# Kernel tuning notes

Measured on AMD Instinct MI355X. Metric: run time of the kernel, lower is better.

## Reference

```python
import jax, jax.numpy as jnp
import numpy as np

B, IMG, PATCH = 32, 128, 8
D, H, L, MLP, NC = 512, 8, 8, 2048, 3
P = (IMG // PATCH) ** 2  # 256 patches
N = P + 1                # +cls token
HD = D // H


def layer_norm(x, g, b, eps=1e-5):
    mu = jnp.mean(x, -1, keepdims=True)
    var = jnp.mean((x - mu) ** 2, -1, keepdims=True)
    return (x - mu) * jax.lax.rsqrt(var + eps) * g + b


def spt(x, w, b, g, beta):
    s = 1
    shifts = [x,
              jnp.roll(x, (s, s), (2, 3)),
              jnp.roll(x, (-s, s), (2, 3)),
              jnp.roll(x, (s, -s), (2, 3)),
              jnp.roll(x, (-s, -s), (2, 3))]
    xs = jnp.concatenate(shifts, axis=1)  # (B,5,H,W)
    y = jax.lax.conv_general_dilated(
        xs, w, (PATCH, PATCH), 'VALID',
        dimension_numbers=('NCHW', 'OIHW', 'NCHW')) + b[None, :, None, None]
    tok = y.reshape(y.shape[0], D, -1).transpose(0, 2, 1)  # (B,P,D)
    return layer_norm(tok, g, beta)


def block(tok, p):
    ln1g, ln1b, qkvw, qkvb, projw, projb, temp, ln2g, ln2b, w1, b1, w2, b2 = p
    x = layer_norm(tok, ln1g, ln1b)
    qkv = (x @ qkvw + qkvb).reshape(x.shape[0], N, 3, H, HD)
    q = jnp.transpose(qkv[:, :, 0], (0, 2, 1, 3))  # (B,H,N,HD)
    k = jnp.transpose(qkv[:, :, 1], (0, 2, 1, 3))
    v = jnp.transpose(qkv[:, :, 2], (0, 2, 1, 3))
    attn = jnp.einsum('bhnd,bhmd->bhnm', q, k) * temp[None, :, None, None]
    attn = jnp.where(jnp.eye(N, dtype=bool)[None, None], -jnp.inf, attn)
    attn = jax.nn.softmax(attn, -1)
    o = jnp.einsum('bhnm,bhmd->bhnd', attn, v)
    o = jnp.transpose(o, (0, 2, 1, 3)).reshape(x.shape[0], N, D)
    tok = tok + o @ projw + projb
    y = layer_norm(tok, ln2g, ln2b)
    y = jax.nn.gelu(y @ w1 + b1, approximate=False) @ w2 + b2
    return tok + y


def setup_inputs() -> dict:
    key = jax.random.key(0)
    ks = jax.random.split(key, 16)
    sc = 0.02
    inp = dict(
        image=jax.random.uniform(ks[0], (B, 1, IMG, IMG), jnp.float32),
        ssw=jax.random.normal(ks[1], (D, 5, PATCH, PATCH), jnp.float32) * sc,
        ssb=jnp.zeros((D,), jnp.float32),
        ssg=jnp.ones((D,), jnp.float32),
        ssbeta=jnp.zeros((D,), jnp.float32),
        sow=jax.random.normal(ks[2], (D, 5, PATCH, PATCH), jnp.float32) * sc,
        sob=jnp.zeros((D,), jnp.float32),
        sog=jnp.ones((D,), jnp.float32),
        sobeta=jnp.zeros((D,), jnp.float32),
        fw=jax.random.normal(ks[3], (2 * D, D), jnp.float32) * sc,
        fb=jnp.zeros((D,), jnp.float32),
        cls_token=jax.random.normal(ks[4], (1, 1, D), jnp.float32) * sc,
        pos_embed=jax.random.normal(ks[5], (1, N, D), jnp.float32) * sc,
        ln1g=jnp.ones((L, D), jnp.float32),
        ln1b=jnp.zeros((L, D), jnp.float32),
        qkvw=jax.random.normal(ks[6], (L, D, 3 * D), jnp.float32) * sc,
        qkvb=jnp.zeros((L, 3 * D), jnp.float32),
        projw=jax.random.normal(ks[7], (L, D, D), jnp.float32) * sc,
        projb=jnp.zeros((L, D), jnp.float32),
        temp=jnp.ones((L, H), jnp.float32) / np.sqrt(HD),
        ln2g=jnp.ones((L, D), jnp.float32),
        ln2b=jnp.zeros((L, D), jnp.float32),
        w1=jax.random.normal(ks[8], (L, D, MLP), jnp.float32) * sc,
        b1=jnp.zeros((L, MLP), jnp.float32),
        w2=jax.random.normal(ks[9], (L, MLP, D), jnp.float32) * sc,
        b2=jnp.zeros((L, D), jnp.float32),
        ng=jnp.ones((D,), jnp.float32),
        nb=jnp.zeros((D,), jnp.float32),
        hw=jax.random.normal(ks[10], (D, NC), jnp.float32) * sc,
        hb=jnp.zeros((NC,), jnp.float32),
    )
    return inp


def reference(image, ssw, ssb, ssg, ssbeta, sow, sob, sog, sobeta, fw, fb,
              cls_token, pos_embed, ln1g, ln1b, qkvw, qkvb, projw, projb,
              temp, ln2g, ln2b, w1, b1, w2, b2, ng, nb, hw, hb):
    # InverseLensLayer is undefined in the source repo snippet: identity
    source = image
    src_tok = spt(source, ssw, ssb, ssg, ssbeta)   # (B,P,D)
    orig_tok = spt(image, sow, sob, sog, sobeta)   # (B,P,D)
    comb = jnp.concatenate([src_tok, orig_tok], -1)
    gate = jax.nn.sigmoid(comb @ fw + fb)
    fused = gate * src_tok + (1.0 - gate) * orig_tok
    cls = jnp.broadcast_to(cls_token, (image.shape[0], 1, D))
    tokens = jnp.concatenate([cls, fused], axis=1) + pos_embed  # (B,N,D)

    def body(tok, p):
        return block(tok, p), None

    params = (ln1g, ln1b, qkvw, qkvb, projw, projb, temp,
              ln2g, ln2b, w1, b1, w2, b2)
    tokens, _ = jax.lax.scan(body, tokens, params)
    cls_out = layer_norm(tokens[:, 0], ng, nb)
    logits = cls_out @ hw + hb
    return logits
```

## Files before the change

kernel.cpp:

```cpp
#include <hip/hip_runtime.h>
#include <math.h>

constexpr int B_ = 32, D_ = 512, H_ = 8, L_ = 8, MLP_ = 2048, NC_ = 3;
constexpr int P_ = 256;
constexpr int N_ = 257;
constexpr int HD_ = 64;
constexpr int BP_ = B_ * P_;
constexpr int BN_ = B_ * N_;
constexpr int MP_ = 8320;
constexpr int KP_ = 320;
constexpr int NV_ = 288;

enum { EPI_BIAS = 0, EPI_RES = 1, EPI_GELU = 2 };

using bf16x8 = __attribute__((ext_vector_type(8))) short;
using f32x4  = __attribute__((ext_vector_type(4))) float;

__device__ __forceinline__ float b2f(unsigned short u) {
    return __uint_as_float(((unsigned)u) << 16);
}
__device__ __forceinline__ unsigned short f2b(float f) {
    unsigned u = __float_as_uint(f);
    unsigned r = (u + 0x7FFFu + ((u >> 16) & 1u)) >> 16;
    return (unsigned short)r;
}

__device__ __forceinline__ void gld_lds16(const void* g, void* l) {
    __builtin_amdgcn_global_load_lds(
        (const __attribute__((address_space(1))) void*)g,
        (__attribute__((address_space(3))) void*)l, 16, 0, 0);
}

__global__ void im2col_k(const float* __restrict__ img,
                         unsigned short* __restrict__ X) {
    int idx = blockIdx.x * 256 + threadIdx.x;
    if (idx >= BP_ * KP_) return;
    int r = idx / KP_, j = idx % KP_;
    int b = r >> 8, p = r & 255;
    int py = p >> 4, px = p & 15;
    int c = j >> 6, kk = j & 63;
    int ky = kk >> 3, kx = kk & 7;
    const int dy[5] = {0, 1, -1, 1, -1};
    const int dx[5] = {0, 1, 1, -1, -1};
    int yy = (py * 8 + ky - dy[c] + 128) & 127;
    int xx = (px * 8 + kx - dx[c] + 128) & 127;
    X[idx] = f2b(img[b * 16384 + yy * 128 + xx]);
}

__global__ __launch_bounds__(256) void castT_k(const float* __restrict__ in,
                                               unsigned short* __restrict__ out,
                                               int K, int N) {
    __shared__ float t[32][33];
    size_t loff = (size_t)blockIdx.z * K * N;
    int k0 = blockIdx.x * 32, n0 = blockIdx.y * 32;
    int tx = threadIdx.x & 31, ty = threadIdx.x >> 5;
    for (int i = ty; i < 32; i += 8)
        t[i][tx] = in[loff + (size_t)(k0 + i) * N + n0 + tx];
    __syncthreads();
    for (int i = ty; i < 32; i += 8)
        out[loff + (size_t)(n0 + i) * K + k0 + tx] = f2b(t[tx][i]);
}

__global__ void cast_k(const float* __restrict__ in,
                       unsigned short* __restrict__ out, int n) {
    int idx = blockIdx.x * 256 + threadIdx.x;
    if (idx < n) out[idx] = f2b(in[idx]);
}

template <int TNT, int NTHR>
__global__ __launch_bounds__(NTHR) void gemm2_k(
    const unsigned short* __restrict__ A, const unsigned short* __restrict__ Bt,
    const float* __restrict__ bias, const float* __restrict__ res,
    float* __restrict__ outF, unsigned short* __restrict__ outB,
    int Nn, int K, int epi) {
    constexpr int BK = 64;
    constexpr int NW = NTHR / 64;
    constexpr int NWC = NW / 2;
    constexpr int ACH = 128 * 8;
    constexpr int BCH = TNT * 8;
    __shared__ unsigned short As[128 * BK];
    __shared__ unsigned short Bs[TNT * BK];
    int tid = threadIdx.x, lane = tid & 63, wave = tid >> 6;
    int quad = lane >> 4, cid = lane & 15;
    int wrow = (wave / NWC) * 64, wcol = (wave % NWC) * 64;
    size_t bm = (size_t)blockIdx.y * 128, bn = (size_t)blockIdx.x * TNT;
    const unsigned short* Ab = A + bm * K;
    const unsigned short* Bb = Bt + bn * K;

    f32x4 acc[4][4] = {};

    for (int k0 = 0; k0 < K; k0 += BK) {
#pragma unroll
        for (int c0 = 0; c0 < ACH; c0 += NTHR) {
            int c = c0 + tid;
            int row = c >> 3, j = c & 7;
            int k8 = j ^ (row & 7);
            int cw = c0 + (tid & ~63);
            gld_lds16(Ab + (size_t)row * K + k0 + k8 * 8,
                      (char*)As + cw * 16);
        }
#pragma unroll
        for (int c0 = 0; c0 < BCH; c0 += NTHR) {
            int c = c0 + tid;
            int row = c >> 3, j = c & 7;
            int k8 = j ^ (row & 7);
            int cw = c0 + (tid & ~63);
            gld_lds16(Bb + (size_t)row * K + k0 + k8 * 8,
                      (char*)Bs + cw * 16);
        }
        __syncthreads();
#pragma unroll
        for (int ks = 0; ks < 2; ++ks) {
            bf16x8 af[4], bfr[4];
#pragma unroll
            for (int i = 0; i < 4; ++i) {
                int r = wrow + i * 16 + cid;
                int j = (ks * 4 + quad) ^ (r & 7);
                af[i] = *(const bf16x8*)&As[(r * 8 + j) * 8];
            }
#pragma unroll
            for (int i = 0; i < 4; ++i) {
                int r = wcol + i * 16 + cid;
                int j = (ks * 4 + quad) ^ (r & 7);
                bfr[i] = *(const bf16x8*)&Bs[(r * 8 + j) * 8];
            }
#pragma unroll
            for (int mi = 0; mi < 4; ++mi)
#pragma unroll
                for (int ni = 0; ni < 4; ++ni)
                    acc[mi][ni] = __builtin_amdgcn_mfma_f32_16x16x32_bf16(
                        af[mi], bfr[ni], acc[mi][ni], 0, 0, 0);
        }
        __syncthreads();
    }

#pragma unroll
    for (int mi = 0; mi < 4; ++mi) {
#pragma unroll
        for (int ni = 0; ni < 4; ++ni) {
            size_t gm0 = bm + wrow + mi * 16 + quad * 4;
            size_t gn = bn + wcol + ni * 16 + cid;
            float bs = bias ? bias[gn] : 0.f;
#pragma unroll
            for (int r = 0; r < 4; ++r) {
                size_t o = (gm0 + r) * Nn + gn;
                float v = acc[mi][ni][r] + bs;
                if (epi == EPI_GELU)
                    v = 0.5f * v * (1.f + erff(v * 0.70710678118654752f));
                else if (epi == EPI_RES)
                    v += res[o];
                if (outF) outF[o] = v;
                if (outB) outB[o] = f2b(v);
            }
        }
    }
}

__global__ __launch_bounds__(256) void ln_k(
    const float* __restrict__ in, float* __restrict__ outF,
    unsigned short* __restrict__ outB, const float* __restrict__ g,
    const float* __restrict__ be, long instride, long ofs, long obs) {
    __shared__ float red[256];
    int row = blockIdx.x;
    const float* x = in + (size_t)row * instride;
    int t = threadIdx.x;
    float v0 = x[t], v1 = x[t + 256];
    red[t] = v0 + v1;
    __syncthreads();
    for (int s = 128; s > 0; s >>= 1) {
        if (t < s) red[t] += red[t + s];
        __syncthreads();
    }
    float mu = red[0] * (1.f / 512.f);
    __syncthreads();
    float d0 = v0 - mu, d1 = v1 - mu;
    red[t] = d0 * d0 + d1 * d1;
    __syncthreads();
    for (int s = 128; s > 0; s >>= 1) {
        if (t < s) red[t] += red[t + s];
        __syncthreads();
    }
    float rs = rsqrtf(red[0] * (1.f / 512.f) + 1e-5f);
    float y0 = d0 * rs * g[t] + be[t];
    float y1 = d1 * rs * g[t + 256] + be[t + 256];
    if (outF) {
        float* y = outF + (size_t)row * ofs;
        y[t] = y0; y[t + 256] = y1;
    }
    if (outB) {
        unsigned short* y = outB + (size_t)row * obs;
        y[t] = f2b(y0); y[t + 256] = f2b(y1);
    }
}

__global__ void assemble_k(const float* __restrict__ gatelin,
                           const float* __restrict__ src,
                           const float* __restrict__ orig,
                           const float* __restrict__ cls,
                           const float* __restrict__ pos,
                           float* __restrict__ tokens) {
    int idx = blockIdx.x * 256 + threadIdx.x;
    if (idx >= B_ * N_ * D_) return;
    int d = idx & 511;
    int bn = idx >> 9;
    int b = bn / N_, n = bn % N_;
    float v;
    if (n == 0) {
        v = cls[d];
    } else {
        int r = b * 256 + (n - 1);
        float gl = gatelin[r * 512 + d];
        float g = 1.f / (1.f + expf(-gl));
        v = g * src[r * 512 + d] + (1.f - g) * orig[r * 512 + d];
    }
    tokens[idx] = v + pos[n * 512 + d];
}

__global__ __launch_bounds__(256) void vT_k(const unsigned short* __restrict__ qkv,
                                            unsigned short* __restrict__ Vt_g) {
    __shared__ unsigned short t[64][72];
    int bh = blockIdx.x, nt = blockIdx.y;
    int b = bh >> 3, h = bh & 7;
    int n0 = nt * 64;
    const unsigned short* vb = qkv + (size_t)(b * N_) * 1536 + 1024 + h * 64;
    int tid = threadIdx.x;
    for (int idx = tid; idx < 64 * 8; idx += 256) {
        int n = idx >> 3, c = idx & 7;
        int gn = n0 + n;
        uint4 u = {0, 0, 0, 0};
        if (gn < N_) u = *(const uint4*)(vb + (size_t)gn * 1536 + c * 8);
        *(uint4*)&t[n][c * 8] = u;
    }
    __syncthreads();
    for (int idx = tid; idx < 64 * 8; idx += 256) {
        int d = idx >> 3, j = idx & 7;
        if (n0 + j * 8 >= NV_) continue;
        unsigned short tmp[8];
#pragma unroll
        for (int e = 0; e < 8; ++e) tmp[e] = t[j * 8 + e][d];
        *(uint4*)&Vt_g[((size_t)bh * 64 + d) * NV_ + n0 + j * 8] =
            *(uint4*)tmp;
    }
}

__global__ __launch_bounds__(256) void attn_fused_k(
    const unsigned short* __restrict__ qkv,
    const unsigned short* __restrict__ Vt_g, const float* __restrict__ temp,
    unsigned short* __restrict__ obuf) {
    __shared__ __align__(16) unsigned short Ps[4][16][40];
    int bh = blockIdx.x;
    int b = bh >> 3, h = bh & 7;
    int tid = threadIdx.x, lane = tid & 63, wave = tid >> 6;
    int quad = lane >> 4, cid = lane & 15;
    int qt = blockIdx.y * 4 + wave;
    if (qt > 16) return;
    const unsigned short* qb = qkv + (size_t)(b * N_) * 1536 + h * 64;
    const unsigned short* kb = qb + 512;
    const unsigned short* vt = Vt_g + (size_t)bh * 64 * NV_;
    float tmp = temp[h];

    int qrow = qt * 16 + cid;
    if (qrow > 256) qrow = 256;
    bf16x8 aq0 = *(const bf16x8*)(qb + (size_t)qrow * 1536 + quad * 8);
    bf16x8 aq1 = *(const bf16x8*)(qb + (size_t)qrow * 1536 + 32 + quad * 8);

    f32x4 s[18];
#pragma unroll
    for (int t = 0; t < 17; ++t) {
        int krow = t * 16 + cid;
        if (t == 16 && krow > 256) krow = 256;
        const unsigned short* kp = kb + (size_t)krow * 1536 + quad * 8;
        bf16x8 bk0 = *(const bf16x8*)kp;
        bf16x8 bk1 = *(const bf16x8*)(kp + 32);
        f32x4 a = {0.f, 0.f, 0.f, 0.f};
        a = __builtin_amdgcn_mfma_f32_16x16x32_bf16(aq0, bk0, a, 0, 0, 0);
        a = __builtin_amdgcn_mfma_f32_16x16x32_bf16(aq1, bk1, a, 0, 0, 0);
        s[t] = a;
    }

    float mx[4] = {-1e30f, -1e30f, -1e30f, -1e30f};
#pragma unroll
    for (int t = 0; t < 17; ++t) {
        int col = t * 16 + cid;
#pragma unroll
        for (int r = 0; r < 4; ++r) {
            int row = qt * 16 + quad * 4 + r;
            float v = s[t][r] * tmp;
            if (col == row || col >= 257) v = -1e30f;
            s[t][r] = v;
            mx[r] = fmaxf(mx[r], v);
        }
    }
    s[17] = f32x4{-1e30f, -1e30f, -1e30f, -1e30f};
#pragma unroll
    for (int m = 1; m < 16; m <<= 1)
#pragma unroll
        for (int r = 0; r < 4; ++r) mx[r] = fmaxf(mx[r], __shfl_xor(mx[r], m));
    float sum[4] = {0.f, 0.f, 0.f, 0.f};
#pragma unroll
    for (int t = 0; t < 18; ++t)
#pragma unroll
        for (int r = 0; r < 4; ++r) {
            float e = __expf(s[t][r] - mx[r]);
            float ef = b2f(f2b(e));
            s[t][r] = ef;
            sum[r] += ef;
        }
#pragma unroll
    for (int m = 1; m < 16; m <<= 1)
#pragma unroll
        for (int r = 0; r < 4; ++r) sum[r] += __shfl_xor(sum[r], m);
    float inv[4];
#pragma unroll
    for (int r = 0; r < 4; ++r) inv[r] = 1.f / sum[r];

    f32x4 o[4] = {};
#pragma unroll
    for (int kt = 0; kt < 9; ++kt) {
#pragma unroll
        for (int hh = 0; hh < 2; ++hh) {
            int t = kt * 2 + hh;
#pragma unroll
            for (int r = 0; r < 4; ++r)
                Ps[wave][quad * 4 + r][hh * 16 + cid] = f2b(s[t][r]);
        }
        bf16x8 ap = *(const bf16x8*)&Ps[wave][cid][quad * 8];
#pragma unroll
        for (int dt = 0; dt < 4; ++dt) {
            bf16x8 bv = *(const bf16x8*)(vt + (size_t)(dt * 16 + cid) * NV_ +
                                         kt * 32 + quad * 8);
            o[dt] =
                __builtin_amdgcn_mfma_f32_16x16x32_bf16(ap, bv, o[dt], 0, 0, 0);
        }
    }
#pragma unroll
    for (int dt = 0; dt < 4; ++dt)
#pragma unroll
        for (int r = 0; r < 4; ++r) {
            int row = qt * 16 + quad * 4 + r;
            if (row < N_)
                obuf[(size_t)(b * N_ + row) * 512 + h * 64 + dt * 16 + cid] =
                    f2b(o[dt][r] * inv[r]);
        }
}

__global__ void head_k(const float* __restrict__ cls_out,
                       const float* __restrict__ hw,
                       const float* __restrict__ hb, float* __restrict__ out) {
    int t = threadIdx.x;
    if (t >= B_ * NC_) return;
    int b = t / NC_, c = t % NC_;
    float acc = hb[c];
    for (int d = 0; d < D_; ++d) acc += cls_out[b * D_ + d] * hw[d * NC_ + c];
    out[t] = acc;
}

extern "C" void kernel_launch(void* const* d_in, const int* in_sizes, int n_in,
                              void* d_out, int out_size, void* d_ws,
                              size_t ws_size, hipStream_t stream) {
    const float* image     = (const float*)d_in[0];
    const float* ssw       = (const float*)d_in[1];
    const float* ssb       = (const float*)d_in[2];
    const float* ssg       = (const float*)d_in[3];
    const float* ssbeta    = (const float*)d_in[4];
    const float* sow       = (const float*)d_in[5];
    const float* sob       = (const float*)d_in[6];
    const float* sog       = (const float*)d_in[7];
    const float* sobeta    = (const float*)d_in[8];
    const float* fw        = (const float*)d_in[9];
    const float* fb        = (const float*)d_in[10];
    const float* cls_token = (const float*)d_in[11];
    const float* pos_embed = (const float*)d_in[12];
    const float* ln1g      = (const float*)d_in[13];
    const float* ln1b      = (const float*)d_in[14];
    const float* qkvw      = (const float*)d_in[15];
    const float* qkvb      = (const float*)d_in[16];
    const float* projw     = (const float*)d_in[17];
    const float* projb     = (const float*)d_in[18];
    const float* temp      = (const float*)d_in[19];
    const float* ln2g      = (const float*)d_in[20];
    const float* ln2b      = (const float*)d_in[21];
    const float* w1        = (const float*)d_in[22];
    const float* b1        = (const float*)d_in[23];
    const float* w2        = (const float*)d_in[24];
    const float* b2        = (const float*)d_in[25];
    const float* ng        = (const float*)d_in[26];
    const float* nb        = (const float*)d_in[27];
    const float* hw        = (const float*)d_in[28];
    const float* hb        = (const float*)d_in[29];
    float* out = (float*)d_out;

    char* w = (char*)d_ws;
    size_t off = 0;
    float* tokens = (float*)w;                           off += (size_t)MP_ * 512 * 4;
    unsigned short* qkvw_t = (unsigned short*)(w + off); off += (size_t)8 * 1536 * 512 * 2;
    unsigned short* projw_t = (unsigned short*)(w + off); off += (size_t)8 * 512 * 512 * 2;
    unsigned short* w1_t = (unsigned short*)(w + off);   off += (size_t)8 * 2048 * 512 * 2;
    unsigned short* w2_t = (unsigned short*)(w + off);   off += (size_t)8 * 512 * 2048 * 2;
    unsigned short* fw_t = (unsigned short*)(w + off);   off += (size_t)512 * 1024 * 2;
    unsigned short* sswb = (unsigned short*)(w + off);   off += (size_t)512 * 320 * 2;
    unsigned short* sowb = (unsigned short*)(w + off);   off += (size_t)512 * 320 * 2;
    char* S = w + off;

    unsigned short* Xb   = (unsigned short*)S;
    float* srct          = (float*)(S + 5242880);
    float* origt         = (float*)(S + 5242880 + 16777216);
    unsigned short* comb = (unsigned short*)(S + 5242880 + 2 * 16777216);
    float* gatelin       = (float*)(S + 5242880 + 3 * 16777216);

    unsigned short* xbuf = (unsigned short*)S;
    unsigned short* qkvB = (unsigned short*)(S + 8519680);
    unsigned short* obuf = (unsigned short*)(S + 8519680 + 25559040);
    unsigned short* hbuf = (unsigned short*)(S + 8519680 + 25559040 + 8519680);
    unsigned short* vt_g = (unsigned short*)(S + 8519680 + 25559040 + 8519680 +
                                             34078720);
    float* cls_out = (float*)(S + 8519680 + 25559040 + 8519680 + 34078720 +
                              9437184);

    castT_k<<<dim3(16, 48, 8), 256, 0, stream>>>(qkvw, qkvw_t, 512, 1536);
    castT_k<<<dim3(16, 16, 8), 256, 0, stream>>>(projw, projw_t, 512, 512);
    castT_k<<<dim3(16, 64, 8), 256, 0, stream>>>(w1, w1_t, 512, 2048);
    castT_k<<<dim3(64, 16, 8), 256, 0, stream>>>(w2, w2_t, 2048, 512);
    castT_k<<<dim3(32, 16, 1), 256, 0, stream>>>(fw, fw_t, 1024, 512);
    cast_k<<<640, 256, 0, stream>>>(ssw, sswb, 512 * 320);
    cast_k<<<640, 256, 0, stream>>>(sow, sowb, 512 * 320);

    im2col_k<<<(BP_ * KP_ + 255) / 256, 256, 0, stream>>>(image, Xb);
    dim3 gspt(4, 64);
    gemm2_k<128, 256><<<gspt, 256, 0, stream>>>(Xb, sswb, ssb, nullptr, srct,
                                                nullptr, 512, KP_, EPI_BIAS);
    ln_k<<<BP_, 256, 0, stream>>>(srct, srct, comb, ssg, ssbeta, 512, 512, 1024);
    gemm2_k<128, 256><<<gspt, 256, 0, stream>>>(Xb, sowb, sob, nullptr, origt,
                                                nullptr, 512, KP_, EPI_BIAS);
    ln_k<<<BP_, 256, 0, stream>>>(origt, origt, comb + 512, sog, sobeta, 512,
                                  512, 1024);
    gemm2_k<128, 256><<<gspt, 256, 0, stream>>>(comb, fw_t, fb, nullptr,
                                                gatelin, nullptr, 512, 1024,
                                                EPI_BIAS);
    assemble_k<<<(B_ * N_ * D_ + 255) / 256, 256, 0, stream>>>(
        gatelin, srct, origt, cls_token, pos_embed, tokens);

    dim3 gqkv(6, 65), gproj(4, 65), gfc1(8, 65), gfc2(4, 65);
    for (int l = 0; l < L_; ++l) {
        const float* l1g = ln1g + l * D_;
        const float* l1b = ln1b + l * D_;
        const unsigned short* qw = qkvw_t + (size_t)l * 1536 * 512;
        const float* qb  = qkvb + (size_t)l * 3 * D_;
        const unsigned short* pw = projw_t + (size_t)l * 512 * 512;
        const float* pb  = projb + (size_t)l * D_;
        const float* tp  = temp + l * H_;
        const float* l2g = ln2g + l * D_;
        const float* l2b = ln2b + l * D_;
        const unsigned short* w1l = w1_t + (size_t)l * 2048 * 512;
        const float* b1l = b1 + (size_t)l * MLP_;
        const unsigned short* w2l = w2_t + (size_t)l * 512 * 2048;
        const float* b2l = b2 + (size_t)l * D_;

        ln_k<<<BN_, 256, 0, stream>>>(tokens, nullptr, xbuf, l1g, l1b, 512, 0,
                                      512);
        gemm2_k<256, 512><<<gqkv, 512, 0, stream>>>(xbuf, qw, qb, nullptr,
                                                    nullptr, qkvB, 1536, 512,
                                                    EPI_BIAS);
        vT_k<<<dim3(256, 5), 256, 0, stream>>>(qkvB, vt_g);
        attn_fused_k<<<dim3(256, 5), 256, 0, stream>>>(qkvB, vt_g, tp, obuf);
        gemm2_k<128, 256><<<gproj, 256, 0, stream>>>(obuf, pw, pb, tokens,
                                                     tokens, nullptr, 512, 512,
                                                     EPI_RES);
        ln_k<<<BN_, 256, 0, stream>>>(tokens, nullptr, xbuf, l2g, l2b, 512, 0,
                                      512);
        gemm2_k<256, 512><<<gfc1, 512, 0, stream>>>(xbuf, w1l, b1l, nullptr,
                                                    nullptr, hbuf, 2048, 512,
                                                    EPI_GELU);
        gemm2_k<128, 256><<<gfc2, 256, 0, stream>>>(hbuf, w2l, b2l, tokens,
                                                    tokens, nullptr, 512, 2048,
                                                    EPI_RES);
    }

    ln_k<<<B_, 256, 0, stream>>>(tokens, cls_out, nullptr, ng, nb,
                                 (long)N_ * 512, 512, 0);
    head_k<<<1, 128, 0, stream>>>(cls_out, hw, hb, out);
}
```

Baseline: 2.559 ms.

## Double-buffer LDS tiles in GEMM and unify on 128x128 tile kernel

Replaces the templated single-buffered GEMM with a 128x128-tile kernel that double-buffers A/B tiles in shared memory, issuing the next tile's global-to-LDS loads before computing the current one and needing only one barrier per k-step. The QKV and FC1 GEMMs move from 256-wide tiles with 512 threads to 128-wide tiles with 256 threads, which doubles their grid sizes. Shared memory per block grows to 64KB, which may limit occupancy. The smaller tiles also give less reuse per block.

```diff
diff --git a/kernel.cpp b/kernel.cpp
--- a/kernel.cpp
+++ b/kernel.cpp
@@ -67,72 +67,84 @@
     if (idx < n) out[idx] = f2b(in[idx]);
 }
 
-template <int TNT, int NTHR>
-__global__ __launch_bounds__(NTHR) void gemm2_k(
+__device__ __forceinline__ void stage_tile(const unsigned short* __restrict__ Ab,
+                                           const unsigned short* __restrict__ Bb,
+                                           int K, int k0,
+                                           unsigned short* As,
+                                           unsigned short* Bs, int tid) {
+#pragma unroll
+    for (int c0 = 0; c0 < 1024; c0 += 256) {
+        int c = c0 + tid;
+        int row = c >> 3, j = c & 7;
+        int k8 = j ^ (row & 7);
+        int cw = c0 + (tid & ~63);
+        gld_lds16(Ab + (size_t)row * K + k0 + k8 * 8, (char*)As + cw * 16);
+    }
+#pragma unroll
+    for (int c0 = 0; c0 < 1024; c0 += 256) {
+        int c = c0 + tid;
+        int row = c >> 3, j = c & 7;
+        int k8 = j ^ (row & 7);
+        int cw = c0 + (tid & ~63);
+        gld_lds16(Bb + (size_t)row * K + k0 + k8 * 8, (char*)Bs + cw * 16);
+    }
+}
+
+__device__ __forceinline__ void compute_tile(const unsigned short* As,
+                                             const unsigned short* Bs,
+                                             int wrow, int wcol, int cid,
+                                             int quad, f32x4 acc[4][4]) {
+#pragma unroll
+    for (int ks = 0; ks < 2; ++ks) {
+        bf16x8 af[4], bfr[4];
+#pragma unroll
+        for (int i = 0; i < 4; ++i) {
+            int r = wrow + i * 16 + cid;
+            int j = (ks * 4 + quad) ^ (r & 7);
+            af[i] = *(const bf16x8*)&As[(r * 8 + j) * 8];
+        }
+#pragma unroll
+        for (int i = 0; i < 4; ++i) {
+            int r = wcol + i * 16 + cid;
+            int j = (ks * 4 + quad) ^ (r & 7);
+            bfr[i] = *(const bf16x8*)&Bs[(r * 8 + j) * 8];
+        }
+#pragma unroll
+        for (int mi = 0; mi < 4; ++mi)
+#pragma unroll
+            for (int ni = 0; ni < 4; ++ni)
+                acc[mi][ni] = __builtin_amdgcn_mfma_f32_16x16x32_bf16(
+                    af[mi], bfr[ni], acc[mi][ni], 0, 0, 0);
+    }
+}
+
+__global__ __launch_bounds__(256) void gemm3_k(
     const unsigned short* __restrict__ A, const unsigned short* __restrict__ Bt,
     const float* __restrict__ bias, const float* __restrict__ res,
     float* __restrict__ outF, unsigned short* __restrict__ outB,
     int Nn, int K, int epi) {
-    constexpr int BK = 64;
-    constexpr int NW = NTHR / 64;
-    constexpr int NWC = NW / 2;
-    constexpr int ACH = 128 * 8;
-    constexpr int BCH = TNT * 8;
-    __shared__ unsigned short As[128 * BK];
-    __shared__ unsigned short Bs[TNT * BK];
+    __shared__ unsigned short As[2][128 * 64];
+    __shared__ unsigned short Bs[2][128 * 64];
     int tid = threadIdx.x, lane = tid & 63, wave = tid >> 6;
     int quad = lane >> 4, cid = lane & 15;
-    int wrow = (wave / NWC) * 64, wcol = (wave % NWC) * 64;
-    size_t bm = (size_t)blockIdx.y * 128, bn = (size_t)blockIdx.x * TNT;
+    int wrow = (wave >> 1) * 64, wcol = (wave & 1) * 64;
+    size_t bm = (size_t)blockIdx.y * 128, bn = (size_t)blockIdx.x * 128;
     const unsigned short* Ab = A + bm * K;
     const unsigned short* Bb = Bt + bn * K;
 
     f32x4 acc[4][4] = {};
-
-    for (int k0 = 0; k0 < K; k0 += BK) {
-#pragma unroll
-        for (int c0 = 0; c0 < ACH; c0 += NTHR) {
-            int c = c0 + tid;
-            int row = c >> 3, j = c & 7;
-            int k8 = j ^ (row & 7);
-            int cw = c0 + (tid & ~63);
-            gld_lds16(Ab + (size_t)row * K + k0 + k8 * 8,
-                      (char*)As + cw * 16);
-        }
-#pragma unroll
-        for (int c0 = 0; c0 < BCH; c0 += NTHR) {
-            int c = c0 + tid;
-            int row = c >> 3, j = c & 7;
-            int k8 = j ^ (row & 7);
-            int cw = c0 + (tid & ~63);
-            gld_lds16(Bb + (size_t)row * K + k0 + k8 * 8,
-                      (char*)Bs + cw * 16);
-        }
+    int nst = K >> 6;
+
+    stage_tile(Ab, Bb, K, 0, As[0], Bs[0], tid);
+    __syncthreads();
+    for (int i = 0; i + 1 < nst; ++i) {
+        int cur = i & 1, nxt = cur ^ 1;
+        stage_tile(Ab, Bb, K, (i + 1) << 6, As[nxt], Bs[nxt], tid);
+        compute_tile(As[cur], Bs[cur], wrow, wcol, cid, quad, acc);
         __syncthreads();
-#pragma unroll
-        for (int ks = 0; ks < 2; ++ks) {
-            bf16x8 af[4], bfr[4];
-#pragma unroll
-            for (int i = 0; i < 4; ++i) {
-                int r = wrow + i * 16 + cid;
-                int j = (ks * 4 + quad) ^ (r & 7);
-                af[i] = *(const bf16x8*)&As[(r * 8 + j) * 8];
-            }
-#pragma unroll
-            for (int i = 0; i < 4; ++i) {
-                int r = wcol + i * 16 + cid;
-                int j = (ks * 4 + quad) ^ (r & 7);
-                bfr[i] = *(const bf16x8*)&Bs[(r * 8 + j) * 8];
-            }
-#pragma unroll
-            for (int mi = 0; mi < 4; ++mi)
-#pragma unroll
-                for (int ni = 0; ni < 4; ++ni)
-                    acc[mi][ni] = __builtin_amdgcn_mfma_f32_16x16x32_bf16(
-                        af[mi], bfr[ni], acc[mi][ni], 0, 0, 0);
-        }
-        __syncthreads();
-    }
+    }
+    compute_tile(As[(nst - 1) & 1], Bs[(nst - 1) & 1], wrow, wcol, cid, quad,
+                 acc);
 
 #pragma unroll
     for (int mi = 0; mi < 4; ++mi) {
@@ -427,20 +439,19 @@
 
     im2col_k<<<(BP_ * KP_ + 255) / 256, 256, 0, stream>>>(image, Xb);
     dim3 gspt(4, 64);
-    gemm2_k<128, 256><<<gspt, 256, 0, stream>>>(Xb, sswb, ssb, nullptr, srct,
-                                                nullptr, 512, KP_, EPI_BIAS);
+    gemm3_k<<<gspt, 256, 0, stream>>>(Xb, sswb, ssb, nullptr, srct, nullptr,
+                                      512, KP_, EPI_BIAS);
     ln_k<<<BP_, 256, 0, stream>>>(srct, srct, comb, ssg, ssbeta, 512, 512, 1024);
-    gemm2_k<128, 256><<<gspt, 256, 0, stream>>>(Xb, sowb, sob, nullptr, origt,
-                                                nullptr, 512, KP_, EPI_BIAS);
+    gemm3_k<<<gspt, 256, 0, stream>>>(Xb, sowb, sob, nullptr, origt, nullptr,
+                                      512, KP_, EPI_BIAS);
     ln_k<<<BP_, 256, 0, stream>>>(origt, origt, comb + 512, sog, sobeta, 512,
                                   512, 1024);
-    gemm2_k<128, 256><<<gspt, 256, 0, stream>>>(comb, fw_t, fb, nullptr,
-                                                gatelin, nullptr, 512, 1024,
-                                                EPI_BIAS);
+    gemm3_k<<<gspt, 256, 0, stream>>>(comb, fw_t, fb, nullptr, gatelin, nullptr,
+                                      512, 1024, EPI_BIAS);
     assemble_k<<<(B_ * N_ * D_ + 255) / 256, 256, 0, stream>>>(
         gatelin, srct, origt, cls_token, pos_embed, tokens);
 
-    dim3 gqkv(6, 65), gproj(4, 65), gfc1(8, 65), gfc2(4, 65);
+    dim3 gqkv(12, 65), gproj(4, 65), gfc1(16, 65), gfc2(4, 65);
     for (int l = 0; l < L_; ++l) {
         const float* l1g = ln1g + l * D_;
         const float* l1b = ln1b + l * D_;
@@ -458,22 +469,18 @@
 
         ln_k<<<BN_, 256, 0, stream>>>(tokens, nullptr, xbuf, l1g, l1b, 512, 0,
                                       512);
-        gemm2_k<256, 512><<<gqkv, 512, 0, stream>>>(xbuf, qw, qb, nullptr,
-                                                    nullptr, qkvB, 1536, 512,
-                                                    EPI_BIAS);
+        gemm3_k<<<gqkv, 256, 0, stream>>>(xbuf, qw, qb, nullptr, nullptr, qkvB,
+                                          1536, 512, EPI_BIAS);
         vT_k<<<dim3(256, 5), 256, 0, stream>>>(qkvB, vt_g);
         attn_fused_k<<<dim3(256, 5), 256, 0, stream>>>(qkvB, vt_g, tp, obuf);
-        gemm2_k<128, 256><<<gproj, 256, 0, stream>>>(obuf, pw, pb, tokens,
-                                                     tokens, nullptr, 512, 512,
-                                                     EPI_RES);
+        gemm3_k<<<gproj, 256, 0, stream>>>(obuf, pw, pb, tokens, tokens,
+                                           nullptr, 512, 512, EPI_RES);
         ln_k<<<BN_, 256, 0, stream>>>(tokens, nullptr, xbuf, l2g, l2b, 512, 0,
                                       512);
-        gemm2_k<256, 512><<<gfc1, 512, 0, stream>>>(xbuf, w1l, b1l, nullptr,
-                                                    nullptr, hbuf, 2048, 512,
-                                                    EPI_GELU);
-        gemm2_k<128, 256><<<gfc2, 256, 0, stream>>>(hbuf, w2l, b2l, tokens,
-                                                    tokens, nullptr, 512, 2048,
-                                                    EPI_RES);
+        gemm3_k<<<gfc1, 256, 0, stream>>>(xbuf, w1l, b1l, nullptr, nullptr,
+                                          hbuf, 2048, 512, EPI_GELU);
+        gemm3_k<<<gfc2, 256, 0, stream>>>(hbuf, w2l, b2l, tokens, tokens,
+                                          nullptr, 512, 2048, EPI_RES);
     }
 
     ln_k<<<B_, 256, 0, stream>>>(tokens, cls_out, nullptr, ng, nb,
```

Result: slower. 2.638 ms (+3.1%).
